# Kernel optimization log

Measured on AMD Instinct MI355X. Metric: run time of the kernel, lower is better.

The kernel has to match this reference:

```python
import jax, jax.numpy as jnp
import numpy as np

GRU_H, H1, H2, ODIM = 256, 128, 64, 3
B, T, HOP = 16, 4000, 80
N = T * HOP  # 320000 samples


def setup_inputs() -> dict:
    key = jax.random.key(0)
    ks = jax.random.split(key, 12)
    inp = {
        'gru_output': jax.random.normal(ks[0], (B, T, GRU_H), dtype=jnp.float32),
        'enhanced': jax.random.normal(ks[1], (B, N), dtype=jnp.float32) * 0.3,
        'noisy': None,
        'W1': jax.random.normal(ks[3], (H1, GRU_H), dtype=jnp.float32) * 0.05,
        'b1': jnp.zeros((H1,), dtype=jnp.float32),
        'a1': jnp.asarray(0.25, dtype=jnp.float32),
        'W2': jax.random.normal(ks[4], (H2, H1), dtype=jnp.float32) * 0.08,
        'b2': jnp.zeros((H2,), dtype=jnp.float32),
        'a2': jnp.asarray(0.25, dtype=jnp.float32),
        'W3': jax.random.normal(ks[5], (ODIM, H2), dtype=jnp.float32) * 0.1,
        'b3': jnp.zeros((ODIM,), dtype=jnp.float32),
    }
    inp['noisy'] = inp['enhanced'] + jax.random.normal(ks[2], (B, N), dtype=jnp.float32) * 0.1
    return inp


def _prelu(x, a):
    return jnp.where(x >= 0, x, a * x)


def _interp_linear(x, n_out):
    # torch F.interpolate(mode='linear', align_corners=False): x [B, T] -> [B, n_out]
    t = x.shape[1]
    src = (jnp.arange(n_out, dtype=jnp.float32) + 0.5) * (t / n_out) - 0.5
    src = jnp.clip(src, 0.0, t - 1)
    i0 = jnp.floor(src).astype(jnp.int32)
    i1 = jnp.minimum(i0 + 1, t - 1)
    w = src - i0.astype(jnp.float32)
    return x[:, i0] * (1.0 - w) + x[:, i1] * w


def _compress(audio, ratio, threshold):
    # soft-knee static gain followed by single-pole IIR smoothing (alpha=0.1)
    env = jnp.abs(audio)
    gain_red = jnp.where(env > threshold, threshold + (env - threshold) / ratio, env)
    gain = jnp.clip(gain_red / (env + 1e-8), 0.1, 2.0)
    alpha = 0.1
    g0 = gain[:, 0]

    def step(carry, g):
        s = alpha * g + (1.0 - alpha) * carry
        return s, s

    _, rest = jax.lax.scan(step, g0, gain[:, 1:].T)  # scan over time, carry [B]
    smoothed = jnp.concatenate([g0[:, None], rest.T], axis=1)
    return audio * smoothed


def reference(gru_output, enhanced, noisy, W1, b1, a1, W2, b2, a2, W3, b3):
    # params MLP (dropout = identity in eval)
    h = _prelu(jnp.einsum('bth,oh->bto', gru_output, W1) + b1, a1)
    h = _prelu(jnp.einsum('bth,oh->bto', h, W2) + b2, a2)
    p = jnp.einsum('bth,oh->bto', h, W3) + b3  # [B, T, 3]

    attack = jax.nn.sigmoid(p[..., 0]) * 0.019 + 0.001
    release = jax.nn.sigmoid(p[..., 1]) * 0.19 + 0.01
    ratio = jnp.clip(jax.nn.softplus(p[..., 2]) + 1.0, 1.0, 20.0)

    n = enhanced.shape[1]
    ratio_i = _interp_linear(ratio, n)
    # attack/release are interpolated in the original but unused by _apply_compression
    _ = _interp_linear(attack, n)
    _ = _interp_linear(release, n)

    residual = noisy - enhanced
    comp_enh = _compress(enhanced, ratio_i, 0.3)
    comp_res = _compress(residual, ratio_i * 0.5, 0.1)

    out = comp_enh + 0.1 * comp_res
    out = out / (jnp.max(jnp.abs(out)) + 1e-8) * jnp.max(jnp.abs(enhanced))
    return out
```

## Files before the change

### kernel.cpp

```cpp
#include <hip/hip_runtime.h>
#include <hip/hip_bf16.h>
#include <math.h>

#define GRU_H 256
#define H1D   128
#define H2D   64
#define BB    16
#define TT    4000
#define NN    320000

typedef __attribute__((ext_vector_type(8))) short short8;
typedef __attribute__((ext_vector_type(4))) float f32x4;

static __device__ __forceinline__ unsigned short f2bf(float x) {
    __bf16 b = (__bf16)x;
    return __builtin_bit_cast(unsigned short, b);
}
static __device__ __forceinline__ float bf2f(unsigned short h) {
    return __uint_as_float(((unsigned)h) << 16);
}
static __device__ __forceinline__ ushort4 cvt4(float4 v) {
    return (ushort4){f2bf(v.x), f2bf(v.y), f2bf(v.z), f2bf(v.w)};
}
static __device__ __forceinline__ short8 cvt_frag(float4 lo, float4 hi) {
    return (short8){(short)f2bf(lo.x), (short)f2bf(lo.y), (short)f2bf(lo.z), (short)f2bf(lo.w),
                    (short)f2bf(hi.x), (short)f2bf(hi.y), (short)f2bf(hi.z), (short)f2bf(hi.w)};
}

#define WS_ESLOT 1024

#define A1CH 2304
__global__ __launch_bounds__(256, 4) void mlp_kernel(
    const float* __restrict__ gru, const float* __restrict__ W1,
    const float* __restrict__ b1,  const float* __restrict__ a1p,
    const float* __restrict__ W2,  const float* __restrict__ b2,
    const float* __restrict__ a2p, const float* __restrict__ W3,
    const float* __restrict__ b3,  float* __restrict__ ratio_out,
    unsigned* __restrict__ ws_u)
{
    __shared__ unsigned short smem[16128];
    __shared__ float w3f[64];
    unsigned short* As  = smem;
    unsigned short* Bs  = smem + 2304;
    unsigned short* h1s = smem + 6912;
    unsigned short* h2s = smem;

    const int t    = threadIdx.x;
    const int wave = t >> 6, lane = t & 63;
    const int lr   = lane & 15, q = lane >> 4;
    const int m0   = blockIdx.x * 64;
    const float a1v = a1p[0], a2v = a2p[0];

    if (blockIdx.x == 0) {
        #pragma unroll
        for (int i = t; i < 2048; i += 256) ws_u[i] = 0u;
    }
    if (t < 64) w3f[t] = W3[2 * H2D + t];

    f32x4 acc1[4][2];
    #pragma unroll
    for (int mi = 0; mi < 4; ++mi)
        #pragma unroll
        for (int ni = 0; ni < 2; ++ni) acc1[mi][ni] = (f32x4){0.f, 0.f, 0.f, 0.f};

    const int arow0 = t >> 3, arow1 = (t + 256) >> 3;
    const int sc4   = t & 7;
    const int brow[4] = { t >> 3, (t + 256) >> 3, (t + 512) >> 3, (t + 768) >> 3 };

    float4 rg[2], rw[4];
    rg[0] = *(const float4*)(gru + (size_t)(m0 + arow0) * GRU_H + sc4 * 4);
    rg[1] = *(const float4*)(gru + (size_t)(m0 + arow1) * GRU_H + sc4 * 4);
    #pragma unroll
    for (int it = 0; it < 4; ++it)
        rw[it] = *(const float4*)(W1 + (size_t)brow[it] * GRU_H + sc4 * 4);

    #pragma unroll 1
    for (int kc = 0; kc < 8; ++kc) {
        __syncthreads();
        *(ushort4*)(As + arow0 * 36 + sc4 * 4) = cvt4(rg[0]);
        *(ushort4*)(As + arow1 * 36 + sc4 * 4) = cvt4(rg[1]);
        #pragma unroll
        for (int it = 0; it < 4; ++it)
            *(ushort4*)(Bs + brow[it] * 36 + sc4 * 4) = cvt4(rw[it]);

        float4 ng[2], nw[4];
        if (kc < 7) {
            const int k1 = (kc + 1) * 32;
            ng[0] = *(const float4*)(gru + (size_t)(m0 + arow0) * GRU_H + k1 + sc4 * 4);
            ng[1] = *(const float4*)(gru + (size_t)(m0 + arow1) * GRU_H + k1 + sc4 * 4);
            #pragma unroll
            for (int it = 0; it < 4; ++it)
                nw[it] = *(const float4*)(W1 + (size_t)brow[it] * GRU_H + k1 + sc4 * 4);
        }
        __syncthreads();

        short8 af[4], bf[2];
        #pragma unroll
        for (int mi = 0; mi < 4; ++mi) {
            const unsigned short* p = As + (mi * 16 + lr) * 36 + q * 8;
            ushort4 lo = *(const ushort4*)(p), hi = *(const ushort4*)(p + 4);
            af[mi] = (short8){(short)lo.x, (short)lo.y, (short)lo.z, (short)lo.w,
                              (short)hi.x, (short)hi.y, (short)hi.z, (short)hi.w};
        }
        #pragma unroll
        for (int ni = 0; ni < 2; ++ni) {
            const unsigned short* p = Bs + (wave * 32 + ni * 16 + lr) * 36 + q * 8;
            ushort4 lo = *(const ushort4*)(p), hi = *(const ushort4*)(p + 4);
            bf[ni] = (short8){(short)lo.x, (short)lo.y, (short)lo.z, (short)lo.w,
                              (short)hi.x, (short)hi.y, (short)hi.z, (short)hi.w};
        }
        #pragma unroll
        for (int mi = 0; mi < 4; ++mi)
            #pragma unroll
            for (int ni = 0; ni < 2; ++ni)
                acc1[mi][ni] = __builtin_amdgcn_mfma_f32_16x16x32_bf16(
                    af[mi], bf[ni], acc1[mi][ni], 0, 0, 0);

        if (kc < 7) {
            rg[0] = ng[0]; rg[1] = ng[1];
            #pragma unroll
            for (int it = 0; it < 4; ++it) rw[it] = nw[it];
        }
    }

    const int col2 = wave * 16 + lr;
    float4 rw2[4][2];
    #pragma unroll
    for (int kc = 0; kc < 4; ++kc) {
        const float* p = W2 + (size_t)col2 * H1D + kc * 32 + q * 8;
        rw2[kc][0] = *(const float4*)(p);
        rw2[kc][1] = *(const float4*)(p + 4);
    }

    #pragma unroll
    for (int ni = 0; ni < 2; ++ni) {
        const int col = wave * 32 + ni * 16 + lr;
        const float bv = b1[col];
        unsigned short* dst = h1s + (col >> 5) * A1CH + (col & 31);
        #pragma unroll
        for (int mi = 0; mi < 4; ++mi) {
            const int rbase = mi * 16 + q * 4;
            #pragma unroll
            for (int r = 0; r < 4; ++r) {
                float x = acc1[mi][ni][r] + bv;
                x = (x >= 0.f) ? x : a1v * x;
                dst[(rbase + r) * 36] = f2bf(x);
            }
        }
    }
    __syncthreads();

    f32x4 acc2[4];
    #pragma unroll
    for (int mi = 0; mi < 4; ++mi) acc2[mi] = (f32x4){0.f, 0.f, 0.f, 0.f};

    #pragma unroll
    for (int kc = 0; kc < 4; ++kc) {
        short8 af[4];
        #pragma unroll
        for (int mi = 0; mi < 4; ++mi) {
            const unsigned short* p = h1s + kc * A1CH + (mi * 16 + lr) * 36 + q * 8;
            ushort4 lo = *(const ushort4*)(p), hi = *(const ushort4*)(p + 4);
            af[mi] = (short8){(short)lo.x, (short)lo.y, (short)lo.z, (short)lo.w,
                              (short)hi.x, (short)hi.y, (short)hi.z, (short)hi.w};
        }
        const short8 bf = cvt_frag(rw2[kc][0], rw2[kc][1]);
        #pragma unroll
        for (int mi = 0; mi < 4; ++mi)
            acc2[mi] = __builtin_amdgcn_mfma_f32_16x16x32_bf16(
                af[mi], bf, acc2[mi], 0, 0, 0);
    }

    {
        const float bv = b2[col2];
        unsigned short* dst = h2s + (col2 >> 5) * A1CH + (col2 & 31);
        #pragma unroll
        for (int mi = 0; mi < 4; ++mi) {
            const int rbase = mi * 16 + q * 4;
            #pragma unroll
            for (int r = 0; r < 4; ++r) {
                float x = acc2[mi][r] + bv;
                x = (x >= 0.f) ? x : a2v * x;
                dst[(rbase + r) * 36] = f2bf(x);
            }
        }
    }
    __syncthreads();

    if (t < 64) {
        float p = b3[2];
        #pragma unroll
        for (int k = 0; k < 64; ++k)
            p = fmaf(bf2f(h2s[(k >> 5) * A1CH + t * 36 + (k & 31)]), w3f[k], p);
        float sp = fmaxf(p, 0.f) + log1pf(expf(-fabsf(p)));
        ratio_out[m0 + t] = fminf(sp + 1.0f, 20.0f);
    }
}

#define CH     256
#define SEGCH  5
#define SEGLEN (CH * SEGCH)
#define SPR    (NN / SEGLEN)
#define NBLK   (BB * SPR / 4)

__global__ __launch_bounds__(256, 4) void compress_kernel(
    const float* __restrict__ enh_g, const float* __restrict__ noi_g,
    const float* __restrict__ ratio, float* __restrict__ out,
    unsigned* __restrict__ ws_u)
{
    const int lane = threadIdx.x & 63;
    const int wid  = blockIdx.x * 4 + (threadIdx.x >> 6);
    const int row  = wid / SPR;
    const int seg  = wid - row * SPR;
    const int s0   = seg * SEGLEN;

    const float* __restrict__ enh  = enh_g + (size_t)row * NN;
    const float* __restrict__ noi  = noi_g + (size_t)row * NN;
    const float* __restrict__ rrow = ratio + row * TT;
    float* __restrict__ orow       = out   + (size_t)row * NN;

    float d_lane = 1.f;
    if (lane & 1)  d_lane *= 0.65610000f;
    if (lane & 2)  d_lane *= 0.43046721f;
    if (lane & 4)  d_lane *= 0.18530202f;
    if (lane & 8)  d_lane *= 0.034336838f;
    if (lane & 16) d_lane *= 0.0011790185f;
    if (lane & 32) d_lane *= 1.3900845e-06f;

    const int p0w = s0 - CH + 4 * lane;
    const int pcw = p0w < 0 ? 0 : p0w;
    float4 e_cur = *(const float4*)(enh + pcw);
    float4 x_cur = *(const float4*)(noi + pcw);

    float s_e = 0.f, s_r = 0.f;
    float amax_c = 0.f, amax_e = 0.f;

    #pragma unroll
    for (int ci = 0; ci < SEGCH + 1; ++ci) {
        float4 e_nxt, x_nxt;
        if (ci < SEGCH) {
            const int pn = s0 - CH + (ci + 1) * CH + 4 * lane;
            e_nxt = *(const float4*)(enh + pn);
            x_nxt = *(const float4*)(noi + pn);
        }

        const int cb = s0 - CH + ci * CH;
        const int p0 = cb + 4 * lane;

        float pe[4], pr[4];
        float ge0 = 0.f, gr0 = 0.f;
        float ae = 0.f, ar = 0.f;
        #pragma unroll
        for (int k = 0; k < 4; ++k) {
            const float e   = (&e_cur.x)[k];
            const float x   = (&x_cur.x)[k];
            const float res = x - e;
            const int n  = p0 + k;
            const int nc = n < 0 ? 0 : n;
            float src = fmaf((float)nc + 0.5f, 0.0125f, -0.5f);
            src = fminf(fmaxf(src, 0.f), 3999.f);
            const int   i0 = (int)src;
            const float w  = src - (float)i0;
            const int   i1 = min(i0 + 1, 3999);
            const float r0 = rrow[i0], r1 = rrow[i1];
            const float rr = r0 * (1.f - w) + r1 * w;
            const float rcp_rr = __builtin_amdgcn_rcpf(rr);

            const float env_e = fabsf(e);
            const float gre = (env_e > 0.3f) ? fmaf(env_e - 0.3f, rcp_rr, 0.3f) : env_e;
            const float ge  = fminf(fmaxf(gre * __builtin_amdgcn_rcpf(env_e + 1e-8f), 0.1f), 2.f);
            const float env_r = fabsf(res);
            const float grr = (env_r > 0.1f) ? fmaf(env_r - 0.1f, 2.f * rcp_rr, 0.1f) : env_r;
            const float gr  = fminf(fmaxf(grr * __builtin_amdgcn_rcpf(env_r + 1e-8f), 0.1f), 2.f);

            if (k == 0) { ge0 = ge; gr0 = gr; }
            ae = fmaf(0.9f, ae, 0.1f * ge);
            ar = fmaf(0.9f, ar, 0.1f * gr);
            pe[k] = ae; pr[k] = ar;
        }

        float Be = pe[3], Br = pr[3];
        #pragma unroll
        for (int l = 0; l < 6; ++l) {
            const int dlt = 1 << l;
            const float ml = (l == 0) ? 0.65610000f  :
                             (l == 1) ? 0.43046721f  :
                             (l == 2) ? 0.18530202f  :
                             (l == 3) ? 0.034336838f :
                             (l == 4) ? 0.0011790185f : 1.3900845e-06f;
            const float me  = (lane >= dlt) ? ml : 0.f;
            const float bse = __shfl_up(Be, dlt, 64);
            const float bsr = __shfl_up(Br, dlt, 64);
            Be = fmaf(me, bse, Be);
            Br = fmaf(me, bsr, Br);
        }
        float Ee = __shfl_up(Be, 1, 64); if (lane == 0) Ee = 0.f;
        float Er = __shfl_up(Br, 1, 64); if (lane == 0) Er = 0.f;

        if (cb == 0) { s_e = __shfl(ge0, 0, 64); s_r = __shfl(gr0, 0, 64); }

        const float Se = fmaf(d_lane, s_e, Ee);
        const float Sr = fmaf(d_lane, s_r, Er);

        if (ci > 0) {
            float4 o;
            #pragma unroll
            for (int k = 0; k < 4; ++k) {
                const float ck = (k == 0) ? 0.9f : (k == 1) ? 0.81f
                               : (k == 2) ? 0.729f : 0.6561f;
                const float sek = fmaf(ck, Se, pe[k]);
                const float srk = fmaf(ck, Sr, pr[k]);
                const float e   = (&e_cur.x)[k];
                const float res = (&x_cur.x)[k] - e;
                const float c   = fmaf(0.1f * res, srk, e * sek);
                (&o.x)[k] = c;
                amax_c = fmaxf(amax_c, fabsf(c));
                amax_e = fmaxf(amax_e, fabsf(e));
            }
            *(float4*)(orow + p0) = o;
        }

        const float b63e = __shfl(Be, 63, 64);
        const float b63r = __shfl(Br, 63, 64);
        s_e = fmaf(1.9287e-12f, s_e, b63e);
        s_r = fmaf(1.9287e-12f, s_r, b63r);
        e_cur = e_nxt; x_cur = x_nxt;
    }

    #pragma unroll
    for (int off = 32; off > 0; off >>= 1) {
        amax_c = fmaxf(amax_c, __shfl_xor(amax_c, off, 64));
        amax_e = fmaxf(amax_e, __shfl_xor(amax_e, off, 64));
    }
    __shared__ float red[8];
    const int wv = threadIdx.x >> 6, ln = threadIdx.x & 63;
    if (ln == 0) { red[wv] = amax_c; red[4 + wv] = amax_e; }
    __syncthreads();
    if (threadIdx.x == 0) {
        float mc = fmaxf(fmaxf(red[0], red[1]), fmaxf(red[2], red[3]));
        float me = fmaxf(fmaxf(red[4], red[5]), fmaxf(red[6], red[7]));
        const int slot = (blockIdx.x & 63) * 16;
        atomicMax(ws_u + slot, __float_as_uint(mc));
        atomicMax(ws_u + WS_ESLOT + slot, __float_as_uint(me));
    }
}

__global__ __launch_bounds__(256) void scale_kernel(float4* __restrict__ out4,
                                                    const unsigned* __restrict__ ws_u)
{
    const int lane = threadIdx.x & 63;
    float vc = __uint_as_float(ws_u[lane * 16]);
    float ve = __uint_as_float(ws_u[WS_ESLOT + lane * 16]);
    #pragma unroll
    for (int off = 32; off > 0; off >>= 1) {
        vc = fmaxf(vc, __shfl_xor(vc, off, 64));
        ve = fmaxf(ve, __shfl_xor(ve, off, 64));
    }
    const float scale = ve / (vc + 1e-8f);
    const size_t i = (size_t)blockIdx.x * 256 + threadIdx.x;
    float4 v = out4[i];
    v.x *= scale; v.y *= scale; v.z *= scale; v.w *= scale;
    out4[i] = v;
}

extern "C" void kernel_launch(void* const* d_in, const int* in_sizes, int n_in,
                              void* d_out, int out_size, void* d_ws, size_t ws_size,
                              hipStream_t stream) {
    const float* gru = (const float*)d_in[0];
    const float* enh = (const float*)d_in[1];
    const float* noi = (const float*)d_in[2];
    const float* W1  = (const float*)d_in[3];
    const float* b1  = (const float*)d_in[4];
    const float* a1  = (const float*)d_in[5];
    const float* W2  = (const float*)d_in[6];
    const float* b2  = (const float*)d_in[7];
    const float* a2  = (const float*)d_in[8];
    const float* W3  = (const float*)d_in[9];
    const float* b3  = (const float*)d_in[10];
    float* out = (float*)d_out;

    unsigned* ws_u = (unsigned*)d_ws;
    float* ratio   = (float*)((char*)d_ws + 8192);

    mlp_kernel<<<(BB * TT) / 64, 256, 0, stream>>>(gru, W1, b1, a1, W2, b2, a2, W3, b3, ratio, ws_u);
    compress_kernel<<<NBLK, 256, 0, stream>>>(enh, noi, ratio, out, ws_u);
    scale_kernel<<<(BB * NN) / 4 / 256, 256, 0, stream>>>((float4*)out, ws_u);
}
```

Before: 174.9 us.

## Pre-convert MLP weights to bf16 and enlarge MLP row tile with double-buffered A

```diff
diff --git a/kernel.cpp b/kernel.cpp
--- a/kernel.cpp
+++ b/kernel.cpp
@@ -22,123 +22,134 @@
 static __device__ __forceinline__ ushort4 cvt4(float4 v) {
     return (ushort4){f2bf(v.x), f2bf(v.y), f2bf(v.z), f2bf(v.w)};
 }
-static __device__ __forceinline__ short8 cvt_frag(float4 lo, float4 hi) {
-    return (short8){(short)f2bf(lo.x), (short)f2bf(lo.y), (short)f2bf(lo.z), (short)f2bf(lo.w),
-                    (short)f2bf(hi.x), (short)f2bf(hi.y), (short)f2bf(hi.z), (short)f2bf(hi.w)};
-}
 
 #define WS_ESLOT 1024
-
-#define A1CH 2304
-__global__ __launch_bounds__(256, 4) void mlp_kernel(
-    const float* __restrict__ gru, const float* __restrict__ W1,
-    const float* __restrict__ b1,  const float* __restrict__ a1p,
-    const float* __restrict__ W2,  const float* __restrict__ b2,
-    const float* __restrict__ a2p, const float* __restrict__ W3,
-    const float* __restrict__ b3,  float* __restrict__ ratio_out,
+#define WS_W1BF_BYTES 270336
+
+__global__ __launch_bounds__(256) void cvt_w_kernel(
+    const float* __restrict__ W1, const float* __restrict__ W2,
+    unsigned short* __restrict__ W1bf, unsigned short* __restrict__ W2bf,
     unsigned* __restrict__ ws_u)
 {
-    __shared__ unsigned short smem[16128];
+    const int t = threadIdx.x;
+    if (blockIdx.x == 0) {
+        #pragma unroll
+        for (int i = t; i < 2048; i += 256) ws_u[i] = 0u;
+    }
+    int idx = (blockIdx.x * 256 + t) * 4;
+    if (idx < 32768) {
+        float4 v = *(const float4*)(W1 + idx);
+        *(ushort4*)(W1bf + idx) = cvt4(v);
+    } else {
+        idx -= 32768;
+        float4 v = *(const float4*)(W2 + idx);
+        *(ushort4*)(W2bf + idx) = cvt4(v);
+    }
+}
+
+#define H1CH 4608
+__global__ __launch_bounds__(256, 2) void mlp_kernel(
+    const float* __restrict__ gru,
+    const unsigned short* __restrict__ W1bf,
+    const float* __restrict__ b1,  const float* __restrict__ a1p,
+    const unsigned short* __restrict__ W2bf,
+    const float* __restrict__ b2,  const float* __restrict__ a2p,
+    const float* __restrict__ W3,  const float* __restrict__ b3,
+    float* __restrict__ ratio_out)
+{
+    __shared__ unsigned short smem[27648];
     __shared__ float w3f[64];
-    unsigned short* As  = smem;
-    unsigned short* Bs  = smem + 2304;
-    unsigned short* h1s = smem + 6912;
+    unsigned short* h1s = smem + 9216;
     unsigned short* h2s = smem;
 
     const int t    = threadIdx.x;
     const int wave = t >> 6, lane = t & 63;
     const int lr   = lane & 15, q = lane >> 4;
-    const int m0   = blockIdx.x * 64;
+    const int m0   = blockIdx.x * 128;
     const float a1v = a1p[0], a2v = a2p[0];
 
-    if (blockIdx.x == 0) {
-        #pragma unroll
-        for (int i = t; i < 2048; i += 256) ws_u[i] = 0u;
-    }
     if (t < 64) w3f[t] = W3[2 * H2D + t];
 
-    f32x4 acc1[4][2];
-    #pragma unroll
-    for (int mi = 0; mi < 4; ++mi)
+    f32x4 acc1[8][2];
+    #pragma unroll
+    for (int mi = 0; mi < 8; ++mi)
         #pragma unroll
         for (int ni = 0; ni < 2; ++ni) acc1[mi][ni] = (f32x4){0.f, 0.f, 0.f, 0.f};
 
-    const int arow0 = t >> 3, arow1 = (t + 256) >> 3;
-    const int sc4   = t & 7;
-    const int brow[4] = { t >> 3, (t + 256) >> 3, (t + 512) >> 3, (t + 768) >> 3 };
-
-    float4 rg[2], rw[4];
-    rg[0] = *(const float4*)(gru + (size_t)(m0 + arow0) * GRU_H + sc4 * 4);
-    rg[1] = *(const float4*)(gru + (size_t)(m0 + arow1) * GRU_H + sc4 * 4);
+    const int srow[4] = { t >> 3, (t + 256) >> 3, (t + 512) >> 3, (t + 768) >> 3 };
+    const int sc4 = t & 7;
+
+    const unsigned short* wbase = W1bf + (size_t)(wave * 32 + lr) * GRU_H + q * 8;
+
+    float4 ra[4];
     #pragma unroll
     for (int it = 0; it < 4; ++it)
-        rw[it] = *(const float4*)(W1 + (size_t)brow[it] * GRU_H + sc4 * 4);
+        ra[it] = *(const float4*)(gru + (size_t)(m0 + srow[it]) * GRU_H + sc4 * 4);
+    short8 bc[2], bn[2];
+    bc[0] = *(const short8*)(wbase);
+    bc[1] = *(const short8*)(wbase + 16 * GRU_H);
+    #pragma unroll
+    for (int it = 0; it < 4; ++it)
+        *(ushort4*)(smem + srow[it] * 36 + sc4 * 4) = cvt4(ra[it]);
+    #pragma unroll
+    for (int it = 0; it < 4; ++it)
+        ra[it] = *(const float4*)(gru + (size_t)(m0 + srow[it]) * GRU_H + 32 + sc4 * 4);
+    bn[0] = *(const short8*)(wbase + 32);
+    bn[1] = *(const short8*)(wbase + 16 * GRU_H + 32);
+    __syncthreads();
 
     #pragma unroll 1
     for (int kc = 0; kc < 8; ++kc) {
-        __syncthreads();
-        *(ushort4*)(As + arow0 * 36 + sc4 * 4) = cvt4(rg[0]);
-        *(ushort4*)(As + arow1 * 36 + sc4 * 4) = cvt4(rg[1]);
-        #pragma unroll
-        for (int it = 0; it < 4; ++it)
-            *(ushort4*)(Bs + brow[it] * 36 + sc4 * 4) = cvt4(rw[it]);
-
-        float4 ng[2], nw[4];
+        unsigned short* Ab = smem + (kc & 1) * 4608;
+        unsigned short* An = smem + ((kc & 1) ^ 1) * 4608;
+
         if (kc < 7) {
-            const int k1 = (kc + 1) * 32;
-            ng[0] = *(const float4*)(gru + (size_t)(m0 + arow0) * GRU_H + k1 + sc4 * 4);
-            ng[1] = *(const float4*)(gru + (size_t)(m0 + arow1) * GRU_H + k1 + sc4 * 4);
             #pragma unroll
             for (int it = 0; it < 4; ++it)
-                nw[it] = *(const float4*)(W1 + (size_t)brow[it] * GRU_H + k1 + sc4 * 4);
-        }
-        __syncthreads();
-
-        short8 af[4], bf[2];
-        #pragma unroll
-        for (int mi = 0; mi < 4; ++mi) {
-            const unsigned short* p = As + (mi * 16 + lr) * 36 + q * 8;
+                *(ushort4*)(An + srow[it] * 36 + sc4 * 4) = cvt4(ra[it]);
+        }
+        short8 bt0, bt1;
+        if (kc < 6) {
+            const int k2 = (kc + 2) * 32;
+            #pragma unroll
+            for (int it = 0; it < 4; ++it)
+                ra[it] = *(const float4*)(gru + (size_t)(m0 + srow[it]) * GRU_H + k2 + sc4 * 4);
+            bt0 = *(const short8*)(wbase + k2);
+            bt1 = *(const short8*)(wbase + 16 * GRU_H + k2);
+        }
+
+        short8 af[8];
+        #pragma unroll
+        for (int mi = 0; mi < 8; ++mi) {
+            const unsigned short* p = Ab + (mi * 16 + lr) * 36 + q * 8;
             ushort4 lo = *(const ushort4*)(p), hi = *(const ushort4*)(p + 4);
             af[mi] = (short8){(short)lo.x, (short)lo.y, (short)lo.z, (short)lo.w,
                               (short)hi.x, (short)hi.y, (short)hi.z, (short)hi.w};
         }
         #pragma unroll
-        for (int ni = 0; ni < 2; ++ni) {
-            const unsigned short* p = Bs + (wave * 32 + ni * 16 + lr) * 36 + q * 8;
-            ushort4 lo = *(const ushort4*)(p), hi = *(const ushort4*)(p + 4);
-            bf[ni] = (short8){(short)lo.x, (short)lo.y, (short)lo.z, (short)lo.w,
-                              (short)hi.x, (short)hi.y, (short)hi.z, (short)hi.w};
-        }
-        #pragma unroll
-        for (int mi = 0; mi < 4; ++mi)
-            #pragma unroll
-            for (int ni = 0; ni < 2; ++ni)
-                acc1[mi][ni] = __builtin_amdgcn_mfma_f32_16x16x32_bf16(
-                    af[mi], bf[ni], acc1[mi][ni], 0, 0, 0);
-
-        if (kc < 7) {
-            rg[0] = ng[0]; rg[1] = ng[1];
-            #pragma unroll
-            for (int it = 0; it < 4; ++it) rw[it] = nw[it];
-        }
+        for (int mi = 0; mi < 8; ++mi) {
+            acc1[mi][0] = __builtin_amdgcn_mfma_f32_16x16x32_bf16(af[mi], bc[0], acc1[mi][0], 0, 0, 0);
+            acc1[mi][1] = __builtin_amdgcn_mfma_f32_16x16x32_bf16(af[mi], bc[1], acc1[mi][1], 0, 0, 0);
+        }
+        bc[0] = bn[0]; bc[1] = bn[1];
+        if (kc < 6) { bn[0] = bt0; bn[1] = bt1; }
+        __syncthreads();
     }
 
     const int col2 = wave * 16 + lr;
-    float4 rw2[4][2];
-    #pragma unroll
-    for (int kc = 0; kc < 4; ++kc) {
-        const float* p = W2 + (size_t)col2 * H1D + kc * 32 + q * 8;
-        rw2[kc][0] = *(const float4*)(p);
-        rw2[kc][1] = *(const float4*)(p + 4);
-    }
+    const unsigned short* w2base = W2bf + (size_t)col2 * H1D + q * 8;
+    short8 b2f[4];
+    #pragma unroll
+    for (int kc = 0; kc < 4; ++kc)
+        b2f[kc] = *(const short8*)(w2base + kc * 32);
 
     #pragma unroll
     for (int ni = 0; ni < 2; ++ni) {
         const int col = wave * 32 + ni * 16 + lr;
         const float bv = b1[col];
-        unsigned short* dst = h1s + (col >> 5) * A1CH + (col & 31);
-        #pragma unroll
-        for (int mi = 0; mi < 4; ++mi) {
+        unsigned short* dst = h1s + (col >> 5) * H1CH + (col & 31);
+        #pragma unroll
+        for (int mi = 0; mi < 8; ++mi) {
             const int rbase = mi * 16 + q * 4;
             #pragma unroll
             for (int r = 0; r < 4; ++r) {
@@ -150,32 +161,31 @@
     }
     __syncthreads();
 
-    f32x4 acc2[4];
-    #pragma unroll
-    for (int mi = 0; mi < 4; ++mi) acc2[mi] = (f32x4){0.f, 0.f, 0.f, 0.f};
+    f32x4 acc2[8];
+    #pragma unroll
+    for (int mi = 0; mi < 8; ++mi) acc2[mi] = (f32x4){0.f, 0.f, 0.f, 0.f};
 
     #pragma unroll
     for (int kc = 0; kc < 4; ++kc) {
-        short8 af[4];
-        #pragma unroll
-        for (int mi = 0; mi < 4; ++mi) {
-            const unsigned short* p = h1s + kc * A1CH + (mi * 16 + lr) * 36 + q * 8;
+        short8 af[8];
+        #pragma unroll
+        for (int mi = 0; mi < 8; ++mi) {
+            const unsigned short* p = h1s + kc * H1CH + (mi * 16 + lr) * 36 + q * 8;
             ushort4 lo = *(const ushort4*)(p), hi = *(const ushort4*)(p + 4);
             af[mi] = (short8){(short)lo.x, (short)lo.y, (short)lo.z, (short)lo.w,
                               (short)hi.x, (short)hi.y, (short)hi.z, (short)hi.w};
         }
-        const short8 bf = cvt_frag(rw2[kc][0], rw2[kc][1]);
-        #pragma unroll
-        for (int mi = 0; mi < 4; ++mi)
+        #pragma unroll
+        for (int mi = 0; mi < 8; ++mi)
             acc2[mi] = __builtin_amdgcn_mfma_f32_16x16x32_bf16(
-                af[mi], bf, acc2[mi], 0, 0, 0);
+                af[mi], b2f[kc], acc2[mi], 0, 0, 0);
     }
 
     {
         const float bv = b2[col2];
-        unsigned short* dst = h2s + (col2 >> 5) * A1CH + (col2 & 31);
-        #pragma unroll
-        for (int mi = 0; mi < 4; ++mi) {
+        unsigned short* dst = h2s + (col2 >> 5) * H1CH + (col2 & 31);
+        #pragma unroll
+        for (int mi = 0; mi < 8; ++mi) {
             const int rbase = mi * 16 + q * 4;
             #pragma unroll
             for (int r = 0; r < 4; ++r) {
@@ -187,11 +197,11 @@
     }
     __syncthreads();
 
-    if (t < 64) {
+    if (t < 128) {
         float p = b3[2];
         #pragma unroll
         for (int k = 0; k < 64; ++k)
-            p = fmaf(bf2f(h2s[(k >> 5) * A1CH + t * 36 + (k & 31)]), w3f[k], p);
+            p = fmaf(bf2f(h2s[(k >> 5) * H1CH + t * 36 + (k & 31)]), w3f[k], p);
         float sp = fmaxf(p, 0.f) + log1pf(expf(-fabsf(p)));
         ratio_out[m0 + t] = fminf(sp + 1.0f, 20.0f);
     }
@@ -381,8 +391,11 @@
 
     unsigned* ws_u = (unsigned*)d_ws;
     float* ratio   = (float*)((char*)d_ws + 8192);
-
-    mlp_kernel<<<(BB * TT) / 64, 256, 0, stream>>>(gru, W1, b1, a1, W2, b2, a2, W3, b3, ratio, ws_u);
+    unsigned short* W1bf = (unsigned short*)((char*)d_ws + WS_W1BF_BYTES);
+    unsigned short* W2bf = W1bf + 32768;
+
+    cvt_w_kernel<<<40, 256, 0, stream>>>(W1, W2, W1bf, W2bf, ws_u);
+    mlp_kernel<<<(BB * TT) / 128, 256, 0, stream>>>(gru, W1bf, b1, a1, W2bf, b2, a2, W3, b3, ratio);
     compress_kernel<<<NBLK, 256, 0, stream>>>(enh, noi, ratio, out, ws_u);
     scale_kernel<<<(BB * NN) / 4 / 256, 256, 0, stream>>>((float4*)out, ws_u);
 }
```

New measurement: 175.2 us. No clear change (+0.1%).
